# Kernel tuning notes

Hardware: AMD Instinct MI355X
Metric: run time of the kernel (lower is better)

The kernel has to match this reference:

```python
import jax, jax.numpy as jnp
import numpy as np

B, N, K = 2, 32768, 16
D_IN, D_OUT = 8, 32
D_HALF = D_OUT // 2
BLOCK = 1024  # query block size for chunked KNN
EPS = 1e-6    # BatchNorm2d eps in the torch module


def _bn(x, g, b):
    # training-mode BatchNorm over all axes except the trailing channel axis
    axes = tuple(range(x.ndim - 1))
    m = jnp.mean(x, axes, keepdims=True)
    v = jnp.var(x, axes, keepdims=True)
    return (x - m) * jax.lax.rsqrt(v + EPS) * g + b


def _knn_idx(coords, k, block=BLOCK):
    # chunked brute-force KNN: never materializes the full (B,N,N) matrix
    b_, n_, _ = coords.shape
    sq = jnp.sum(coords * coords, -1)  # (B,N)
    q = coords.reshape(b_, n_ // block, block, 3).transpose(1, 0, 2, 3)
    q2 = sq.reshape(b_, n_ // block, block).transpose(1, 0, 2)

    def f(args):
        qi, q2i = args  # (B,block,3), (B,block)
        d = q2i[..., None] + sq[:, None, :] - 2.0 * jnp.einsum('bqc,bnc->bqn', qi, coords)
        return jax.lax.top_k(-d, k)[1]  # (B,block,k) nearest indices

    idx = jax.lax.map(f, (q, q2))  # (nb,B,block,k)
    return idx.transpose(1, 0, 2, 3).reshape(b_, n_, k)


def _lse(coords, feats, idx, Wl, bl, g, b):
    # coords (B,N,3), feats (B,N,C), idx (B,N,K) -> (B,N,K,2C)
    neigh = jax.vmap(lambda c, i: c[i])(coords, idx)            # (B,N,K,3)
    center = jnp.broadcast_to(coords[:, :, None, :], neigh.shape)
    ones = jnp.ones(idx.shape + (1,), coords.dtype)             # torch passes idx only -> dist=1
    cat = jnp.concatenate([center, neigh, center - neigh, ones], -1)  # (B,N,K,10)
    h = jax.nn.relu(_bn(cat @ Wl.T + bl, g, b))                 # (B,N,K,C)
    fexp = jnp.broadcast_to(feats[:, :, None, :], h.shape)
    return jnp.concatenate([h, fexp], -1)


def _attpool(x, Ws, Wp, bp, g, b):
    # x (B,N,K,Cin) -> (B,N,Cout); softmax over K (torch dim=-2 after permute)
    s = jax.nn.softmax(x @ Ws.T, axis=2)
    f = jnp.sum(s * x, 2)                                       # (B,N,Cin)
    return jax.nn.relu(_bn(f @ Wp.T + bp, g, b))


def setup_inputs() -> dict:
    key = jax.random.key(0)
    ks = iter(jax.random.split(key, 40))
    p = lambda *s: jax.random.normal(next(ks), s, jnp.float32) * 0.1
    d = {
        'coords': jax.random.normal(next(ks), (B, N, 3), jnp.float32) * 10.0,
        'features': jax.random.normal(next(ks), (B, D_IN, N, 1), jnp.float32),
        'W1': p(D_HALF, D_IN), 'b1': p(D_HALF),
        'Wl1': p(D_HALF, 10), 'bl1': p(D_HALF),
        'gl1': jnp.ones((D_HALF,), jnp.float32), 'bl1b': jnp.zeros((D_HALF,), jnp.float32),
        'Ws1': p(D_OUT, D_OUT),
        'Wp1': p(D_HALF, D_OUT), 'bp1': p(D_HALF),
        'gp1': jnp.ones((D_HALF,), jnp.float32), 'bp1b': jnp.zeros((D_HALF,), jnp.float32),
        'Wl2': p(D_HALF, 10), 'bl2': p(D_HALF),
        'gl2': jnp.ones((D_HALF,), jnp.float32), 'bl2b': jnp.zeros((D_HALF,), jnp.float32),
        'Ws2': p(D_OUT, D_OUT),
        'Wp2': p(D_OUT, D_OUT), 'bp2': p(D_OUT),
        'gp2': jnp.ones((D_OUT,), jnp.float32), 'bp2b': jnp.zeros((D_OUT,), jnp.float32),
        'W2': p(2 * D_OUT, D_OUT), 'b2': p(2 * D_OUT),
        'Wsc': p(2 * D_OUT, D_IN), 'bsc': p(2 * D_OUT),
        'gsc': jnp.ones((2 * D_OUT,), jnp.float32), 'bscb': jnp.zeros((2 * D_OUT,), jnp.float32),
    }
    return d


def reference(coords, features, W1, b1, Wl1, bl1, gl1, bl1b, Ws1, Wp1, bp1, gp1, bp1b,
              Wl2, bl2, gl2, bl2b, Ws2, Wp2, bp2, gp2, bp2b, W2, b2, Wsc, bsc, gsc, bscb):
    feats = features[:, :, :, 0].transpose(0, 2, 1)             # (B,N,d_in) channel-last
    idx = _knn_idx(jax.lax.stop_gradient(coords), K)            # (B,N,K)
    x = jax.nn.leaky_relu(feats @ W1.T + b1, 0.2)               # mlp1 -> (B,N,d_out/2)
    x = _lse(coords, x, idx, Wl1, bl1, gl1, bl1b)               # (B,N,K,d_out)
    x = _attpool(x, Ws1, Wp1, bp1, gp1, bp1b)                   # (B,N,d_out/2)
    x = _lse(coords, x, idx, Wl2, bl2, gl2, bl2b)               # (B,N,K,d_out)
    x = _attpool(x, Ws2, Wp2, bp2, gp2, bp2b)                   # (B,N,d_out)
    out = x @ W2.T + b2                                         # mlp2 -> (B,N,2*d_out)
    sc = _bn(feats @ Wsc.T + bsc, gsc, bscb)                    # shortcut with BN
    out = jax.nn.leaky_relu(out + sc, 0.01)
    return out.transpose(0, 2, 1)[..., None]                    # (B,2*d_out,N,1)
```

## Files before the change

### kernel.cpp

```cpp
#include <hip/hip_runtime.h>
#include <math.h>

#define NPTS  32768
#define NB    2
#define NQ    (NB*NPTS)
#define KK    16
#define EPS   1e-6f
#define G     16
#define G3    (G*G*G)
#define HB    2048
#define SLOP  0.05f
#define TEPS  1e-3f
#define CAPC  512
#define CAP2  1408
#define INVQK (1.f/(float)((size_t)NQ*KK))
#define INVN  (1.f/(float)NQ)

#define S_L1 0
#define S_L2 32
#define S_P1 64
#define S_P2 96
#define S_SC 160

#define WS_X1     (NQ*16)
#define WS_T2     (NQ*32)
#define WS_T4     (NQ*48)
#define WS_STAT   (NQ*80)
#define WS_COEF   (WS_STAT + 512)
#define WS_GCNT   (WS_STAT + 1024)
#define WS_GSTART (WS_GCNT + 2*G3)
#define WS_CELLID (WS_GSTART + 2*G3)
#define WS_SORTID (WS_CELLID + NQ)
#define WS_CSORT  (WS_SORTID + NQ)
#define WS_BBOX   (WS_CSORT + 4*NQ)
#define WS_HIST   (WS_BBOX + 16)
#define WS_EDGE   (WS_HIST + 6*HB)
#define WS_STARTS WS_HIST
#define WS_FAIL   WS_CELLID
#define WS_PART   WS_CSORT
#define WS_PARTA  WS_T2

#define FB_BAD    (1 << 30)

__device__ __forceinline__ float wred64(float v) {
#pragma unroll
  for (int m = 32; m > 0; m >>= 1) v += __shfl_xor(v, m, 64);
  return v;
}

__device__ __forceinline__ unsigned int encf(float f) {
  unsigned int u = __float_as_uint(f);
  return (u & 0x80000000u) ? ~u : (u | 0x80000000u);
}
__device__ __forceinline__ float decf(unsigned int u) {
  return (u & 0x80000000u) ? __uint_as_float(u & 0x7fffffffu) : __uint_as_float(~u);
}

__device__ __forceinline__ int bs16(const float* e, float x) {
  int c = (x >= e[8]) ? 8 : 0;
  c += (x >= e[c+4]) ? 4 : 0;
  c += (x >= e[c+2]) ? 2 : 0;
  c += (x >= e[c+1]) ? 1 : 0;
  return c;
}

__global__ void k_zero_all(float* __restrict__ stats, int* __restrict__ gcnt,
                           int* __restrict__ hist, unsigned int* __restrict__ bbox,
                           int* __restrict__ failcnt) {
  int i = blockIdx.x*256 + threadIdx.x;
  if (i < 2*G3) gcnt[i] = 0;
  if (i < 6*HB) hist[i] = 0;
  if (i < 320)  stats[i] = 0.f;
  if (i < 12)   bbox[i] = ((i % 6) < 3) ? 0xFFFFFFFFu : 0u;
  if (i == 0)   failcnt[0] = 0;
}

__global__ void k_pred(const float* __restrict__ part, int nblk, int nch,
                       float* __restrict__ stats, int soff) {
  __shared__ float red[256];
  int c = blockIdx.x, tid = threadIdx.x;
  float s = 0.f;
  for (int i = tid; i < nblk; i += 256) s += part[(size_t)i*nch + c];
  red[tid] = s;
  __syncthreads();
  for (int off2 = 128; off2 > 0; off2 >>= 1) {
    if (tid < off2) red[tid] += red[tid + off2];
    __syncthreads();
  }
  if (tid == 0) stats[soff + c] = red[0];
}

__global__ void k_pred2(const float* __restrict__ pa, const float* __restrict__ pb,
                        float* __restrict__ stats) {
  __shared__ float red[256];
  int cb = blockIdx.x, tid = threadIdx.x;
  const float* part; int nblk, nch, soff, c;
  if (cb < 128) { part = pa; nblk = 64;   nch = 128; soff = S_SC; c = cb; }
  else          { part = pb; nblk = 1024; nch = 64;  soff = S_L1; c = cb - 128; }
  float s = 0.f;
  for (int i = tid; i < nblk; i += 256) s += part[(size_t)i*nch + c];
  red[tid] = s;
  __syncthreads();
  for (int off2 = 128; off2 > 0; off2 >>= 1) {
    if (tid < off2) red[tid] += red[tid + off2];
    __syncthreads();
  }
  if (tid == 0) stats[soff + c] = red[0];
}

__global__ void k_bbox(const float* __restrict__ coords, unsigned int* __restrict__ bbox) {
  __shared__ unsigned int rmn[3][4], rmx[3][4];
  int tid = threadIdx.x;
  int t = blockIdx.x*256 + tid;
  int b = t >> 15, n = t & (NPTS-1);
  const float* cb = coords + (size_t)b*(NPTS*3);
  unsigned int e[3] = { encf(cb[n*3+0]), encf(cb[n*3+1]), encf(cb[n*3+2]) };
  unsigned int mn[3] = { e[0], e[1], e[2] }, mx[3] = { e[0], e[1], e[2] };
#pragma unroll
  for (int s = 32; s > 0; s >>= 1) {
#pragma unroll
    for (int a = 0; a < 3; ++a) {
      unsigned int o1 = (unsigned int)__shfl_xor((int)mn[a], s, 64);
      unsigned int o2 = (unsigned int)__shfl_xor((int)mx[a], s, 64);
      mn[a] = mn[a] < o1 ? mn[a] : o1;
      mx[a] = mx[a] > o2 ? mx[a] : o2;
    }
  }
  int wave = tid >> 6, lane = tid & 63;
  if (lane == 0) {
#pragma unroll
    for (int a = 0; a < 3; ++a) { rmn[a][wave] = mn[a]; rmx[a][wave] = mx[a]; }
  }
  __syncthreads();
  if (tid < 3) {
    unsigned int a0 = min(min(rmn[tid][0], rmn[tid][1]), min(rmn[tid][2], rmn[tid][3]));
    unsigned int A0 = max(max(rmx[tid][0], rmx[tid][1]), max(rmx[tid][2], rmx[tid][3]));
    atomicMin(&bbox[b*6 + tid], a0);
    atomicMax(&bbox[b*6 + 3 + tid], A0);
  }
}

__global__ void k_hist(const float* __restrict__ coords, const unsigned int* __restrict__ bbox,
                       int* __restrict__ hist) {
  int t = blockIdx.x*256 + threadIdx.x;
  int b = t >> 15, n = t & (NPTS-1);
  const float* cb = coords + (size_t)b*(NPTS*3);
#pragma unroll
  for (int a = 0; a < 3; ++a) {
    float l = decf(bbox[b*6+a]), h = decf(bbox[b*6+3+a]);
    float ex = (h - l)*(1.f + 4e-7f) + 1e-30f;
    float inv = (float)HB/ex;
    int bin = (int)((cb[n*3+a] - l)*inv);
    bin = min(HB-1, max(0, bin));
    atomicAdd(&hist[(b*3+a)*HB + bin], 1);
  }
}

__global__ void k_edges(const int* __restrict__ hist, const unsigned int* __restrict__ bbox,
                        float* __restrict__ edges) {
  __shared__ int part[256];
  int p = blockIdx.x;
  int b = p/3, a = p - b*3;
  int tid = threadIdx.x;
  const int* h = hist + p*HB;
  int v[8]; int s = 0;
#pragma unroll
  for (int i = 0; i < 8; ++i) { v[i] = h[tid*8 + i]; s += v[i]; }
  part[tid] = s;
  __syncthreads();
  for (int off = 1; off < 256; off <<= 1) {
    int x = part[tid];
    int y = (tid >= off) ? part[tid-off] : 0;
    __syncthreads();
    part[tid] = x + y;
    __syncthreads();
  }
  float l = decf(bbox[b*6+a]), hi = decf(bbox[b*6+3+a]);
  float ex = (hi - l)*(1.f + 4e-7f) + 1e-30f;
  float bw = ex*(1.f/(float)HB);
  int c = part[tid] - s;
#pragma unroll
  for (int i = 0; i < 8; ++i) {
    int lo_c = c; c += v[i];
#pragma unroll
    for (int g = 1; g < G; ++g) {
      int tq = g*(NPTS/G);
      if (lo_c < tq && c >= tq) edges[p*(G+1) + g] = l + bw*(float)(tid*8 + i + 1);
    }
  }
  if (tid == 0) { edges[p*(G+1)] = l; edges[p*(G+1) + G] = hi + fabsf(hi)*1e-6f + 1e-20f; }
}

__global__ void k_bin(const float* __restrict__ coords, const float* __restrict__ edges,
                      int* __restrict__ cellid, int* __restrict__ gcnt) {
  __shared__ float se[3][G+1];
  int tid = threadIdx.x;
  int t = blockIdx.x*256 + tid;
  int b = t >> 15, n = t & (NPTS-1);
  if (tid < 3*(G+1)) se[tid/(G+1)][tid%(G+1)] = edges[b*3*(G+1) + tid];
  __syncthreads();
  const float* cb = coords + (size_t)b*(NPTS*3);
  int c0 = bs16(se[0], cb[n*3+0]);
  int c1 = bs16(se[1], cb[n*3+1]);
  int c2 = bs16(se[2], cb[n*3+2]);
  int cid = b*G3 + (c2*G + c1)*G + c0;
  cellid[t] = cid;
  atomicAdd(&gcnt[cid], 1);
}

__global__ void k_alloc(const int* __restrict__ gcnt, int* __restrict__ gstart,
                        int* __restrict__ starts) {
  __shared__ int part[1024];
  int tid = threadIdx.x;
  int v[8]; int s = 0;
#pragma unroll
  for (int i = 0; i < 8; ++i) { v[i] = gcnt[tid*8 + i]; s += v[i]; }
  part[tid] = s;
  __syncthreads();
  for (int off = 1; off < 1024; off <<= 1) {
    int x = part[tid];
    int y = (tid >= off) ? part[tid-off] : 0;
    __syncthreads();
    part[tid] = x + y;
    __syncthreads();
  }
  int base = part[tid] - s;
#pragma unroll
  for (int i = 0; i < 8; ++i) { gstart[tid*8 + i] = base; starts[tid*8 + i] = base; base += v[i]; }
  if (tid == 1023) starts[2*G3] = NQ;
}

__global__ void k_scatter(const float* __restrict__ coords, const int* __restrict__ cellid,
                          int* __restrict__ gstart, float4* __restrict__ csort,
                          int* __restrict__ sortid) {
  int t = blockIdx.x*256 + threadIdx.x;
  int b = t >> 15, n = t & (NPTS-1);
  const float* cb = coords + (size_t)b*(NPTS*3);
  int cid = cellid[t];
  int pos = atomicAdd(&gstart[cid], 1);
  float x = cb[n*3+0], y = cb[n*3+1], z = cb[n*3+2];
  csort[pos] = make_float4(x, y, z, x*x + y*y + z*z);
  sortid[pos] = n;
}

__launch_bounds__(256)
__global__ void k_cellknn(const float4* __restrict__ csort, const int* __restrict__ sortid,
                          const int* __restrict__ starts, const float* __restrict__ edges,
                          int* __restrict__ oidx, int* __restrict__ faillist,
                          int* __restrict__ failcnt) {
  __shared__ float4 big[CAP2];
  __shared__ float  sbdA[4][64];
  __shared__ int    sbiA[4][64];
  __shared__ int    rs[9], rl[9], pre[10];
  __shared__ int    rs2[25], rl2[25], pre2[26];
  __shared__ int    nfl[4];
  __shared__ int    flq[4][16];
  __shared__ float  flT[4][16];
  int tid = threadIdx.x, lane = tid & 63, w = tid >> 6;
  int blk = blockIdx.x;
  int b = blk >> 12;
  int c = blk & (G3-1);
  int cxi = c & 15, cyi = (c >> 4) & 15, czi = c >> 8;
  const int* st = starts + b*G3;
  float* sbd = &sbdA[w][0];
  int*   sbi = &sbiA[w][0];
  if (tid < 4) nfl[tid] = 0;
  if (tid < 9) {
    int dz = tid/3 - 1, dy = tid%3 - 1;
    int z = czi + dz, y = cyi + dy;
    if (z < 0 || z > G-1 || y < 0 || y > G-1) { rs[tid] = 0; rl[tid] = 0; }
    else {
      int xa = max(cxi-1, 0), xb = min(cxi+1, G-1);
      int c0 = (z*G + y)*G + xa;
      int s0 = st[c0], e0 = st[c0 + (xb - xa) + 1];
      rs[tid] = s0; rl[tid] = e0 - s0;
    }
  }
  __syncthreads();
  if (tid == 0) {
    int acc = 0;
#pragma unroll
    for (int i = 0; i < 9; ++i) { pre[i] = acc; acc += rl[i]; }
    pre[9] = acc;
  }
  __syncthreads();
  int total = pre[9];
  int hs = st[c], he = st[c+1];
  int nq = he - hs;
  if (nq == 0) return;
  bool bad = (total > CAPC) || (total < KK);
  if (!bad) {
    for (int i = tid; i < total; i += 256) {
      int row = 0;
#pragma unroll
      for (int rr = 1; rr < 9; ++rr) row += (i >= pre[rr]);
      int gp = rs[row] + (i - pre[row]);
      big[i] = csort[gp];
    }
  }
  __syncthreads();
  int hoff = pre[4] + (hs - rs[4]);
  float blo[3], bhi[3]; bool blok[3], bhik[3];
  int cc3[3] = {cxi, cyi, czi};
#pragma unroll
  for (int a = 0; a < 3; ++a) {
    const float* e = edges + (b*3 + a)*(G+1);
    blok[a] = cc3[a] > 0;     blo[a] = blok[a] ? e[cc3[a]-1] : 0.f;
    bhik[a] = cc3[a] < G-1;   bhi[a] = bhik[a] ? e[cc3[a]+2] : 0.f;
  }
  for (int q0 = 0; q0 < nq; q0 += 4) {
    int qi = q0 + w;
    if (qi >= nq) continue;
    int t = hs + qi;
    if (bad) {
      if (lane == 0) { int pos = atomicAdd(failcnt, 1); faillist[pos] = t | FB_BAD; }
      continue;
    }
    float4 qv = big[hoff + qi];
    float qx = qv.x, qy = qv.y, qz = qv.z, qsq = qv.w;
    float dreg[8];
#pragma unroll
    for (int s = 0; s < 8; ++s) {
      int i = s*64 + lane;
      float d = 1e30f;
      if (i < total) {
        float4 p = big[i];
        d = qsq + p.w - 2.f*(qx*p.x + qy*p.y + qz*p.z);
      }
      dreg[s] = d;
    }
    float mnl = fminf(fminf(fminf(dreg[0],dreg[1]), fminf(dreg[2],dreg[3])),
                      fminf(fminf(dreg[4],dreg[5]), fminf(dreg[6],dreg[7])));
    float v = mnl;
#pragma unroll
    for (int k2 = 2; k2 <= 64; k2 <<= 1) {
#pragma unroll
      for (int j = k2 >> 1; j > 0; j >>= 1) {
        float o = __shfl_xor(v, j, 64);
        bool keepmin = (((lane & j) == 0) == ((lane & k2) == 0));
        v = keepmin ? fminf(v, o) : fmaxf(v, o);
      }
    }
    float Tp = __shfl(v, 15, 64);
    int cnt = 0;
#pragma unroll
    for (int s = 0; s < 8; ++s) {
      bool take = dreg[s] <= Tp;
      unsigned long long bal = __ballot(take);
      int pos = cnt + __popcll(bal & ((1ull << lane) - 1ull));
      if (take && pos < 64) { sbd[pos] = dreg[s]; sbi[pos] = s*64 + lane; }
      cnt += __popcll(bal);
    }
    if (cnt > 64) {
      if (lane == 0) { int pos = atomicAdd(failcnt, 1); faillist[pos] = t | FB_BAD; }
      continue;
    }
    float dv = (lane < cnt) ? sbd[lane] : 1e30f;
    int   iv = (lane < cnt) ? sbi[lane] : 0x7fffffff;
    if (cnt <= 32) {
#pragma unroll
      for (int kk = 2; kk <= 32; kk <<= 1) {
#pragma unroll
        for (int j = kk >> 1; j > 0; j >>= 1) {
          float od = __shfl_xor(dv, j, 64);
          int   oi = __shfl_xor(iv, j, 64);
          bool keepmin = (((lane & j) == 0) == ((lane & kk) == 0));
          bool less = (od < dv) || (od == dv && oi < iv);
          bool take2 = keepmin ? less : !less;
          dv = take2 ? od : dv;
          iv = take2 ? oi : iv;
        }
      }
    } else {
#pragma unroll
      for (int kk = 2; kk <= 64; kk <<= 1) {
#pragma unroll
        for (int j = kk >> 1; j > 0; j >>= 1) {
          float od = __shfl_xor(dv, j, 64);
          int   oi = __shfl_xor(iv, j, 64);
          bool keepmin = (((lane & j) == 0) == ((lane & kk) == 0));
          bool less = (od < dv) || (od == dv && oi < iv);
          bool take2 = keepmin ? less : !less;
          dv = take2 ? od : dv;
          iv = take2 ? oi : iv;
        }
      }
    }
    float d16v = __shfl(dv, 15, 64);
    int resid = iv;
    float m = 1e30f;
    if (blok[0]) m = fminf(m, qx - blo[0]);
    if (bhik[0]) m = fminf(m, bhi[0] - qx);
    if (blok[1]) m = fminf(m, qy - blo[1]);
    if (bhik[1]) m = fminf(m, bhi[1] - qy);
    if (blok[2]) m = fminf(m, qz - blo[2]);
    if (bhik[2]) m = fminf(m, bhi[2] - qz);
    bool ok = (m > 0.f) && (m*m > d16v + SLOP);
    if (ok) {
      int qn = sortid[t];
      size_t row = ((size_t)(b*NPTS + qn))*KK;
      if (lane < KK) {
        int rowi = 0;
#pragma unroll
        for (int rr = 1; rr < 9; ++rr) rowi += (resid >= pre[rr]);
        int gp = rs[rowi] + (resid - pre[rowi]);
        oidx[row + lane] = sortid[gp];
      }
    } else {
      if (lane == 0) {
        int k2 = nfl[w];
        if (k2 < 16) { flq[w][k2] = t; flT[w][k2] = d16v; nfl[w] = k2 + 1; }
        else { int pos = atomicAdd(failcnt, 1); faillist[pos] = t | FB_BAD; }
      }
    }
  }
  __syncthreads();
  if (bad) return;
  if (nfl[0] + nfl[1] + nfl[2] + nfl[3] == 0) return;

  if (tid < 25) {
    int dz = tid/5 - 2, dy = tid%5 - 2;
    int z = czi + dz, y = cyi + dy;
    if (z < 0 || z > G-1 || y < 0 || y > G-1) { rs2[tid] = 0; rl2[tid] = 0; }
    else {
      int xa = max(cxi-2, 0), xb = min(cxi+2, G-1);
      int c0 = (z*G + y)*G + xa;
      int s0 = st[c0], e0 = st[c0 + (xb - xa) + 1];
      rs2[tid] = s0; rl2[tid] = e0 - s0;
    }
  }
  __syncthreads();
  if (tid == 0) {
    int acc = 0;
#pragma unroll
    for (int i = 0; i < 25; ++i) { pre2[i] = acc; acc += rl2[i]; }
    pre2[25] = acc;
  }
  __syncthreads();
  int total2 = pre2[25];
  if (total2 > CAP2) {
    if (lane == 0) {
      for (int k2 = 0; k2 < nfl[w]; ++k2) {
        int pos = atomicAdd(failcnt, 1); faillist[pos] = flq[w][k2] | FB_BAD;
      }
    }
    return;
  }
  for (int i = tid; i < total2; i += 256) {
    int rowi = 0;
#pragma unroll
    for (int rr = 1; rr < 25; ++rr) rowi += (i >= pre2[rr]);
    int gp = rs2[rowi] + (i - pre2[rowi]);
    big[i] = csort[gp];
  }
  __syncthreads();
  float blo2[3], bhi2[3]; bool blok2[3], bhik2[3];
#pragma unroll
  for (int a = 0; a < 3; ++a) {
    const float* e = edges + (b*3 + a)*(G+1);
    blok2[a] = cc3[a] > 1;     blo2[a] = blok2[a] ? e[cc3[a]-2] : 0.f;
    bhik2[a] = cc3[a] < G-2;   bhi2[a] = bhik2[a] ? e[cc3[a]+3] : 0.f;
  }
  for (int k2 = 0; k2 < nfl[w]; ++k2) {
    int t = flq[w][k2];
    float T0 = flT[w][k2] + TEPS;
    float4 qv = csort[t];
    float qx = qv.x, qy = qv.y, qz = qv.z, qsq = qv.w;
    int cnt = 0;
    for (int base2 = 0; base2 < total2; base2 += 64) {
      int i = base2 + lane;
      bool valid = i < total2;
      float d = 1e30f;
      if (valid) {
        float4 p = big[i];
        d = qsq + p.w - 2.f*(qx*p.x + qy*p.y + qz*p.z);
      }
      bool take = valid && (d <= T0);
      unsigned long long bal = __ballot(take);
      int pos = cnt + __popcll(bal & ((1ull << lane) - 1ull));
      if (take && pos < 64) { sbd[pos] = d; sbi[pos] = i; }
      cnt += __popcll(bal);
    }
    if (cnt > 64) {
      if (lane == 0) { int pos = atomicAdd(failcnt, 1); faillist[pos] = t | FB_BAD; }
      continue;
    }
    float dv = (lane < cnt) ? sbd[lane] : 1e30f;
    int   iv = (lane < cnt) ? sbi[lane] : 0x7fffffff;
#pragma unroll
    for (int kk = 2; kk <= 64; kk <<= 1) {
#pragma unroll
      for (int j = kk >> 1; j > 0; j >>= 1) {
        float od = __shfl_xor(dv, j, 64);
        int   oi = __shfl_xor(iv, j, 64);
        bool keepmin = (((lane & j) == 0) == ((lane & kk) == 0));
        bool less = (od < dv) || (od == dv && oi < iv);
        bool take2 = keepmin ? less : !less;
        dv = take2 ? od : dv;
        iv = take2 ? oi : iv;
      }
    }
    float d16b = __shfl(dv, 15, 64);
    float m = 1e30f;
    if (blok2[0]) m = fminf(m, qx - blo2[0]);
    if (bhik2[0]) m = fminf(m, bhi2[0] - qx);
    if (blok2[1]) m = fminf(m, qy - blo2[1]);
    if (bhik2[1]) m = fminf(m, bhi2[1] - qy);
    if (blok2[2]) m = fminf(m, qz - blo2[2]);
    if (bhik2[2]) m = fminf(m, bhi2[2] - qz);
    bool ok = (m > 0.f) && (m*m > d16b + SLOP);
    int qn = sortid[t];
    size_t row = ((size_t)(b*NPTS + qn))*KK;
    if (lane < KK) {
      int rowi = 0;
#pragma unroll
      for (int rr = 1; rr < 25; ++rr) rowi += (iv >= pre2[rr]);
      int gp = rs2[rowi] + (iv - pre2[rowi]);
      oidx[row + lane] = ok ? sortid[gp] : gp;
    }
    if (!ok && lane == 0) { int pos = atomicAdd(failcnt, 1); faillist[pos] = t; }
  }
}

__launch_bounds__(256)
__global__ void k_knn_fb(const float4* __restrict__ csort, const int* __restrict__ sortid,
                         const int* __restrict__ starts, const float* __restrict__ edges,
                         const int* __restrict__ faillist, const int* __restrict__ failcnt,
                         int* __restrict__ oidx) {
  int tid = threadIdx.x, lane = tid & 63, w = tid >> 6;
  int gw = blockIdx.x*4 + w, nw = gridDim.x*4;
  int nf = failcnt[0];
  for (int f = gw; f < nf; f += nw) {
    int fv = faillist[f];
    bool seeded = (fv & FB_BAD) == 0;
    int t = fv & (FB_BAD - 1);
    int b = t >> 15;
    const int* st = starts + b*G3;
    const float* ex = edges + (b*3+0)*(G+1);
    const float* ey = edges + (b*3+1)*(G+1);
    const float* ez = edges + (b*3+2)*(G+1);
    float4 qv = csort[t];
    const float qx = qv.x, qy = qv.y, qz = qv.z, qsq = qv.w;
    int qn = sortid[t];
    size_t row = ((size_t)(b*NPTS + qn))*KK;
    float T;
    int lo_pos, hi_pos;
    if (seeded) {
      float sd = -1e30f;
      if (lane < KK) {
        int pos = oidx[row + lane];
        float4 p = csort[pos];
        sd = qsq + p.w - 2.f*(qx*p.x + qy*p.y + qz*p.z);
      }
      T = sd;
#pragma unroll
      for (int m = 32; m > 0; m >>= 1) T = fmaxf(T, __shfl_xor(T, m, 64));
      T += TEPS;
      float R = sqrtf(T)*1.0001f + 1e-12f;
      bool tk = (lane < G-1) && (ex[lane+1] < qx - R);
      int xl = __popcll(__ballot(tk));
      tk = (lane >= 1 && lane <= G-1) && (ex[lane] > qx + R);
      int xh = (G-1) - __popcll(__ballot(tk));
      tk = (lane < G-1) && (ey[lane+1] < qy - R);
      int yl = __popcll(__ballot(tk));
      tk = (lane >= 1 && lane <= G-1) && (ey[lane] > qy + R);
      int yh = (G-1) - __popcll(__ballot(tk));
      tk = (lane < G-1) && (ez[lane+1] < qz - R);
      int zl = __popcll(__ballot(tk));
      tk = (lane >= 1 && lane <= G-1) && (ez[lane] > qz + R);
      int zh = (G-1) - __popcll(__ballot(tk));
      lo_pos = st[(zl*G + yl)*G + xl];
      hi_pos = st[(zh*G + yh)*G + xh + 1];
    } else {
      float mn = 1e30f;
      for (int i = b*NPTS + lane; i < b*NPTS + NPTS; i += 64) {
        float4 p = csort[i];
        float d = qsq + p.w - 2.f*(qx*p.x + qy*p.y + qz*p.z);
        mn = fminf(mn, d);
      }
      float v = mn;
#pragma unroll
      for (int k2 = 2; k2 <= 64; k2 <<= 1) {
#pragma unroll
        for (int j = k2 >> 1; j > 0; j >>= 1) {
          float o = __shfl_xor(v, j, 64);
          bool keepmin = (((lane & j) == 0) == ((lane & k2) == 0));
          v = keepmin ? fminf(v, o) : fmaxf(v, o);
        }
      }
      T = __shfl(v, 15, 64) + TEPS;
      lo_pos = b*NPTS;
      hi_pos = b*NPTS + NPTS;
    }
    float dl[KK]; int il[KK];
#pragma unroll
    for (int i = 0; i < KK; ++i) { dl[i] = 1e30f; il[i] = 0x7fffffff; }
    for (int i = lo_pos + lane; i < hi_pos; i += 64) {
      float4 p = csort[i];
      float d = qsq + p.w - 2.f*(qx*p.x + qy*p.y + qz*p.z);
      if (d <= T && d < dl[KK-1]) {
        float cd = d; int ci = i;
#pragma unroll
        for (int i2 = 0; i2 < KK; ++i2) {
          bool sw = cd < dl[i2];
          float td = dl[i2]; int ti = il[i2];
          dl[i2] = sw ? cd : td; il[i2] = sw ? ci : ti;
          cd = sw ? td : cd;    ci = sw ? ti : ci;
        }
      }
    }
    int res = 0;
#pragma unroll
    for (int r = 0; r < KK; ++r) {
      float v = dl[0]; int pi = il[0]; int l = lane;
#pragma unroll
      for (int m = 1; m < 64; m <<= 1) {
        float ov = __shfl_xor(v, m, 64);
        int   op = __shfl_xor(pi, m, 64);
        int   ol = __shfl_xor(l, m, 64);
        bool take = (ov < v) || (ov == v && op < pi);
        v = take ? ov : v; pi = take ? op : pi; l = take ? ol : l;
      }
      if (lane == r) res = pi;
      bool win = (lane == l);
#pragma unroll
      for (int i = 0; i < KK-1; ++i) {
        dl[i] = win ? dl[i+1] : dl[i];
        il[i] = win ? il[i+1] : il[i];
      }
      dl[KK-1] = win ? 1e30f : dl[KK-1];
      il[KK-1] = win ? 0x7fffffff : il[KK-1];
    }
    if (lane < KK) oidx[row + lane] = sortid[res];
  }
}

__global__ void k_stats(const float* __restrict__ features,
                        const float* __restrict__ W1, const float* __restrict__ b1,
                        const float* __restrict__ Wsc, const float* __restrict__ bsc,
                        float* __restrict__ x1, float* __restrict__ ppa,
                        const float* __restrict__ coords, const int* __restrict__ idx,
                        const float* __restrict__ Wl1, const float* __restrict__ bl1,
                        const float* __restrict__ Wl2, const float* __restrict__ bl2,
                        float* __restrict__ ppb) {
  int tid = threadIdx.x;
  if (blockIdx.x < 64) {
    __shared__ float sW1[128], sb1[16], sWsc[512], sbsc[64];
    __shared__ float part[128];
    if (tid < 128) { sW1[tid] = W1[tid]; part[tid] = 0.f; }
    if (tid < 16)  sb1[tid] = b1[tid];
    if (tid < 64)  sbsc[tid] = bsc[tid];
    for (int i = tid; i < 512; i += 256) sWsc[i] = Wsc[i];
    __syncthreads();
    int q0 = blockIdx.x*1024;
    float f[4][8];
#pragma unroll
    for (int p = 0; p < 4; ++p) {
      int q = q0 + p*256 + tid;
      int b = q >> 15, n = q & (NPTS-1);
#pragma unroll
      for (int c = 0; c < 8; ++c) f[p][c] = features[((size_t)b*8 + c)*NPTS + n];
#pragma unroll
      for (int co = 0; co < 16; ++co) {
        float a = sb1[co];
#pragma unroll
        for (int c = 0; c < 8; ++c) a += f[p][c]*sW1[co*8+c];
        x1[(size_t)q*16 + co] = a > 0.f ? a : 0.2f*a;
      }
    }
    int lane = tid & 63;
#pragma unroll
    for (int co = 0; co < 64; ++co) {
      float s = 0.f, ss = 0.f;
#pragma unroll
      for (int p = 0; p < 4; ++p) {
        float a = sbsc[co];
#pragma unroll
        for (int c = 0; c < 8; ++c) a += f[p][c]*sWsc[co*8+c];
        s += a; ss += a*a;
      }
      s = wred64(s); ss = wred64(ss);
      if (lane == 0) { atomicAdd(&part[co], s); atomicAdd(&part[64+co], ss); }
    }
    __syncthreads();
    if (tid < 128) ppa[(size_t)blockIdx.x*128 + tid] = part[tid];
  } else {
    __shared__ float sW1[160], sb1[16], sW2[160], sb2[16];
    __shared__ float red[4][64];
    int blk = blockIdx.x - 64;
    for (int i = tid; i < 160; i += 256) { sW1[i] = Wl1[i]; sW2[i] = Wl2[i]; }
    if (tid < 16) { sb1[tid] = bl1[tid]; sb2[tid] = bl2[tid]; }
    __syncthreads();
    float cat[4][10];
#pragma unroll
    for (int p = 0; p < 4; ++p) {
      int t = blk*1024 + p*256 + tid;
      int q = t >> 4;
      int b = q >> 15, n = q & (NPTS-1);
      const float* cb = coords + (size_t)b*(NPTS*3);
      int j = idx[t];
      float cx = cb[n*3], cy = cb[n*3+1], cz = cb[n*3+2];
      float px = cb[j*3], py = cb[j*3+1], pz = cb[j*3+2];
      cat[p][0]=cx; cat[p][1]=cy; cat[p][2]=cz;
      cat[p][3]=px; cat[p][4]=py; cat[p][5]=pz;
      cat[p][6]=cx-px; cat[p][7]=cy-py; cat[p][8]=cz-pz; cat[p][9]=1.f;
    }
    int wave = tid >> 6, lane = tid & 63;
#pragma unroll
    for (int co = 0; co < 16; ++co) {
      float s1 = 0.f, q1 = 0.f, s2 = 0.f, q2 = 0.f;
#pragma unroll
      for (int p = 0; p < 4; ++p) {
        float a1 = sb1[co], a2 = sb2[co];
#pragma unroll
        for (int d0 = 0; d0 < 10; ++d0) { a1 += cat[p][d0]*sW1[co*10+d0]; a2 += cat[p][d0]*sW2[co*10+d0]; }
        s1 += a1; q1 += a1*a1; s2 += a2; q2 += a2*a2;
      }
      s1 = wred64(s1); q1 = wred64(q1);
      s2 = wred64(s2); q2 = wred64(q2);
      if (lane == 0) { red[wave][co]=s1; red[wave][16+co]=q1; red[wave][32+co]=s2; red[wave][48+co]=q2; }
    }
    __syncthreads();
    if (tid < 64) {
      float v = red[0][tid] + red[1][tid] + red[2][tid] + red[3][tid];
      ppb[(size_t)blk*64 + tid] = v;
    }
  }
}

__launch_bounds__(256)
__global__ void k_att1(const float* __restrict__ coords, const int* __restrict__ idx,
                       const float* __restrict__ x1ws,
                       const float* __restrict__ Wl1, const float* __restrict__ bl1,
                       const float* __restrict__ Ws1, const float* __restrict__ Wp1,
                       const float* __restrict__ bp1, const float* __restrict__ stats,
                       const float* __restrict__ gl1, const float* __restrict__ bl1b,
                       float* __restrict__ t2, float* __restrict__ ppart) {
  __shared__ float saL[16], scL[16];
  __shared__ float sWl[160], sbl[16];
  __shared__ float sWs[1024];
  __shared__ float sWpT[512], sbp[16];
  __shared__ float lsum[16], lsq[16];
  int tid = threadIdx.x;
  if (tid < 16) {
    float m = stats[S_L1 + tid]*INVQK;
    float v = stats[S_L1 + 16 + tid]*INVQK - m*m;
    float a = gl1[tid]*rsqrtf(v + EPS);
    saL[tid] = a; scL[tid] = bl1b[tid] - m*a;
  }
  __syncthreads();
  for (int i = tid; i < 160; i += 256) { int c = i/10; sWl[i] = Wl1[i]*saL[c]; }
  if (tid < 16) sbl[tid] = bl1[tid]*saL[tid] + scL[tid];
  for (int i = tid; i < 1024; i += 256) sWs[i] = Ws1[i];
  for (int i = tid; i < 512; i += 256) { int co = i >> 4, cp = i & 15; sWpT[i] = Wp1[cp*32 + co]; }
  if (tid < 16) { sbp[tid] = bp1[tid]; lsum[tid] = 0.f; lsq[tid] = 0.f; }
  __syncthreads();
  int gp = blockIdx.x*16 + (tid >> 4);
  int k  = tid & 15;
  int b = gp >> 15, n = gp & (NPTS-1);
  const float* cb = coords + (size_t)b*(NPTS*3);
  int j = idx[(size_t)gp*KK + k];
  float cx = cb[n*3], cy = cb[n*3+1], cz = cb[n*3+2];
  float px = cb[j*3], py = cb[j*3+1], pz = cb[j*3+2];
  float cat[10] = {cx,cy,cz,px,py,pz,cx-px,cy-py,cz-pz,1.f};
  float x[32];
#pragma unroll
  for (int co = 0; co < 16; ++co) {
    float a = sbl[co];
#pragma unroll
    for (int d0 = 0; d0 < 10; ++d0) a += cat[d0]*sWl[co*10+d0];
    x[co] = a > 0.f ? a : 0.f;
  }
  {
    const float4* xp = (const float4*)(x1ws + (size_t)gp*16);
    float4 u0 = xp[0], u1 = xp[1], u2 = xp[2], u3 = xp[3];
    x[16]=u0.x; x[17]=u0.y; x[18]=u0.z; x[19]=u0.w;
    x[20]=u1.x; x[21]=u1.y; x[22]=u1.z; x[23]=u1.w;
    x[24]=u2.x; x[25]=u2.y; x[26]=u2.z; x[27]=u2.w;
    x[28]=u3.x; x[29]=u3.y; x[30]=u3.z; x[31]=u3.w;
  }
  float tacc = sbp[k];
#pragma unroll
  for (int co = 0; co < 32; ++co) {
    float s = 0.f;
#pragma unroll
    for (int ci = 0; ci < 32; ++ci) s += x[ci]*sWs[co*32+ci];
    float e = __expf(s);
    float se = e;
#pragma unroll
    for (int msk = 8; msk > 0; msk >>= 1) se += __shfl_xor(se, msk, 16);
    float w = e/se;
    float fv = w*x[co];
#pragma unroll
    for (int msk = 8; msk > 0; msk >>= 1) fv += __shfl_xor(fv, msk, 16);
    tacc += fv*sWpT[co*16+k];
  }
  t2[(size_t)gp*16 + k] = tacc;
  atomicAdd(&lsum[k], tacc);
  atomicAdd(&lsq[k], tacc*tacc);
  __syncthreads();
  if (tid < 16) {
    ppart[(size_t)blockIdx.x*32 + tid]      = lsum[tid];
    ppart[(size_t)blockIdx.x*32 + 16 + tid] = lsq[tid];
  }
}

__launch_bounds__(256)
__global__ void k_att2(const float* __restrict__ coords, const int* __restrict__ idx,
                       const float* __restrict__ t2ws,
                       const float* __restrict__ Wl2, const float* __restrict__ bl2,
                       const float* __restrict__ Ws2, const float* __restrict__ Wp2,
                       const float* __restrict__ bp2, const float* __restrict__ stats,
                       const float* __restrict__ gl2, const float* __restrict__ bl2b,
                       const float* __restrict__ gp1, const float* __restrict__ bp1b,
                       float* __restrict__ t4, float* __restrict__ ppart) {
  __shared__ float saL[16], scL[16];
  __shared__ float sWl[160], sbl[16];
  __shared__ float sWs[1024];
  __shared__ float sWpT[1024], sbp[32];
  __shared__ float sa1[16], sc1[16];
  __shared__ float lsum[32], lsq[32];
  int tid = threadIdx.x;
  if (tid < 16) {
    float m = stats[S_L2 + tid]*INVQK;
    float v = stats[S_L2 + 16 + tid]*INVQK - m*m;
    float a = gl2[tid]*rsqrtf(v + EPS);
    saL[tid] = a; scL[tid] = bl2b[tid] - m*a;
    float m1 = stats[S_P1 + tid]*INVN;
    float v1 = stats[S_P1 + 16 + tid]*INVN - m1*m1;
    float a1 = gp1[tid]*rsqrtf(v1 + EPS);
    sa1[tid] = a1; sc1[tid] = bp1b[tid] - m1*a1;
  }
  __syncthreads();
  for (int i = tid; i < 160; i += 256) { int c = i/10; sWl[i] = Wl2[i]*saL[c]; }
  if (tid < 16) sbl[tid] = bl2[tid]*saL[tid] + scL[tid];
  for (int i = tid; i < 1024; i += 256) {
    sWs[i] = Ws2[i];
    int co = i >> 5, cp = i & 31; sWpT[i] = Wp2[cp*32 + co];
  }
  if (tid < 32) { sbp[tid] = bp2[tid]; lsum[tid]=0.f; lsq[tid]=0.f; }
  __syncthreads();
  int gp = blockIdx.x*16 + (tid >> 4);
  int k  = tid & 15;
  int b = gp >> 15, n = gp & (NPTS-1);
  const float* cb = coords + (size_t)b*(NPTS*3);
  int j = idx[(size_t)gp*KK + k];
  float cx = cb[n*3], cy = cb[n*3+1], cz = cb[n*3+2];
  float px = cb[j*3], py = cb[j*3+1], pz = cb[j*3+2];
  float cat[10] = {cx,cy,cz,px,py,pz,cx-px,cy-py,cz-pz,1.f};
  float x[32];
#pragma unroll
  for (int co = 0; co < 16; ++co) {
    float a = sbl[co];
#pragma unroll
    for (int d0 = 0; d0 < 10; ++d0) a += cat[d0]*sWl[co*10+d0];
    x[co] = a > 0.f ? a : 0.f;
  }
  {
    const float4* xp = (const float4*)(t2ws + (size_t)gp*16);
    float4 u0 = xp[0], u1 = xp[1], u2 = xp[2], u3 = xp[3];
    float xv[16] = {u0.x,u0.y,u0.z,u0.w, u1.x,u1.y,u1.z,u1.w,
                    u2.x,u2.y,u2.z,u2.w, u3.x,u3.y,u3.z,u3.w};
#pragma unroll
    for (int c = 0; c < 16; ++c) {
      float v = xv[c]*sa1[c] + sc1[c];
      x[16+c] = v > 0.f ? v : 0.f;
    }
  }
  float tacc0 = sbp[k], tacc1 = sbp[k+16];
#pragma unroll
  for (int co = 0; co < 32; ++co) {
    float s = 0.f;
#pragma unroll
    for (int ci = 0; ci < 32; ++ci) s += x[ci]*sWs[co*32+ci];
    float e = __expf(s);
    float se = e;
#pragma unroll
    for (int msk = 8; msk > 0; msk >>= 1) se += __shfl_xor(se, msk, 16);
    float w = e/se;
    float fv = w*x[co];
#pragma unroll
    for (int msk = 8; msk > 0; msk >>= 1) fv += __shfl_xor(fv, msk, 16);
    tacc0 += fv*sWpT[co*32+k];
    tacc1 += fv*sWpT[co*32+k+16];
  }
  t4[(size_t)gp*32 + k]      = tacc0;
  t4[(size_t)gp*32 + k + 16] = tacc1;
  atomicAdd(&lsum[k], tacc0);      atomicAdd(&lsq[k], tacc0*tacc0);
  atomicAdd(&lsum[k+16], tacc1);   atomicAdd(&lsq[k+16], tacc1*tacc1);
  __syncthreads();
  if (tid < 32) {
    ppart[(size_t)blockIdx.x*64 + tid]      = lsum[tid];
    ppart[(size_t)blockIdx.x*64 + 32 + tid] = lsq[tid];
  }
}

__global__ void k_final(const float* __restrict__ t4ws, const float* __restrict__ features,
                        const float* __restrict__ W2, const float* __restrict__ b2,
                        const float* __restrict__ Wsc, const float* __restrict__ bsc,
                        const float* __restrict__ stats,
                        const float* __restrict__ gsc, const float* __restrict__ bscb,
                        const float* __restrict__ gp2, const float* __restrict__ bp2b,
                        float* __restrict__ out) {
  __shared__ float saS[64], scS[64];
  __shared__ float sW2[2048], sb2[64], sWscF[512], sbscF[64], sa[32], scc[32];
  int tid = threadIdx.x;
  if (tid < 64) {
    float m = stats[S_SC + tid]*INVN;
    float v = stats[S_SC + 64 + tid]*INVN - m*m;
    float a = gsc[tid]*rsqrtf(v + EPS);
    saS[tid] = a; scS[tid] = bscb[tid] - m*a;
  }
  if (tid < 32) {
    float m = stats[S_P2 + tid]*INVN;
    float v = stats[S_P2 + 32 + tid]*INVN - m*m;
    float a = gp2[tid]*rsqrtf(v + EPS);
    sa[tid] = a; scc[tid] = bp2b[tid] - m*a;
  }
  __syncthreads();
  for (int i = tid; i < 2048; i += 256) sW2[i] = W2[i];
  if (tid < 64) sb2[tid] = b2[tid];
  for (int i = tid; i < 512; i += 256) { int c2 = i >> 3; sWscF[i] = Wsc[i]*saS[c2]; }
  if (tid < 64) sbscF[tid] = bsc[tid]*saS[tid] + scS[tid];
  __syncthreads();
  int q = blockIdx.x*256 + tid;
  int b = q >> 15, n = q & (NPTS-1);
  float x3[32];
  const float4* tp = (const float4*)(t4ws + (size_t)q*32);
#pragma unroll
  for (int i = 0; i < 8; ++i) {
    float4 u = tp[i];
    float v0 = u.x*sa[4*i+0] + scc[4*i+0];
    float v1 = u.y*sa[4*i+1] + scc[4*i+1];
    float v2 = u.z*sa[4*i+2] + scc[4*i+2];
    float v3 = u.w*sa[4*i+3] + scc[4*i+3];
    x3[4*i+0] = v0 > 0.f ? v0 : 0.f;
    x3[4*i+1] = v1 > 0.f ? v1 : 0.f;
    x3[4*i+2] = v2 > 0.f ? v2 : 0.f;
    x3[4*i+3] = v3 > 0.f ? v3 : 0.f;
  }
  float f[8];
#pragma unroll
  for (int c = 0; c < 8; ++c) f[c] = features[((size_t)b*8+c)*NPTS + n];
  for (int c2 = 0; c2 < 64; ++c2) {
    float acc = sb2[c2];
#pragma unroll
    for (int co = 0; co < 32; ++co) acc += x3[co]*sW2[c2*32+co];
    float sv = sbscF[c2];
#pragma unroll
    for (int c = 0; c < 8; ++c) sv += f[c]*sWscF[c2*8+c];
    float o = acc + sv;
    out[((size_t)b*64 + c2)*NPTS + n] = o > 0.f ? o : 0.01f*o;
  }
}

extern "C" void kernel_launch(void* const* d_in, const int* in_sizes, int n_in,
                              void* d_out, int out_size, void* d_ws, size_t ws_size,
                              hipStream_t stream) {
  const float* coords   = (const float*)d_in[0];
  const float* features = (const float*)d_in[1];
  const float* W1  = (const float*)d_in[2];
  const float* b1  = (const float*)d_in[3];
  const float* Wl1 = (const float*)d_in[4];
  const float* bl1 = (const float*)d_in[5];
  const float* gl1 = (const float*)d_in[6];
  const float* bl1b= (const float*)d_in[7];
  const float* Ws1 = (const float*)d_in[8];
  const float* Wp1 = (const float*)d_in[9];
  const float* bp1 = (const float*)d_in[10];
  const float* gp1 = (const float*)d_in[11];
  const float* bp1b= (const float*)d_in[12];
  const float* Wl2 = (const float*)d_in[13];
  const float* bl2 = (const float*)d_in[14];
  const float* gl2 = (const float*)d_in[15];
  const float* bl2b= (const float*)d_in[16];
  const float* Ws2 = (const float*)d_in[17];
  const float* Wp2 = (const float*)d_in[18];
  const float* bp2 = (const float*)d_in[19];
  const float* gp2 = (const float*)d_in[20];
  const float* bp2b= (const float*)d_in[21];
  const float* W2  = (const float*)d_in[22];
  const float* b2  = (const float*)d_in[23];
  const float* Wsc = (const float*)d_in[24];
  const float* bsc = (const float*)d_in[25];
  const float* gsc = (const float*)d_in[26];
  const float* bscb= (const float*)d_in[27];

  float* wsF  = (float*)d_ws;
  int*   wsI  = (int*)d_ws;
  int*   idxp = wsI;
  float* x1p  = wsF + WS_X1;
  float* t2p  = wsF + WS_T2;
  float* t4p  = wsF + WS_T4;
  float* stat = wsF + WS_STAT;
  int*   gcnt = wsI + WS_GCNT;
  int*   gsta = wsI + WS_GSTART;
  int*   gcel = wsI + WS_CELLID;
  int*   sid  = wsI + WS_SORTID;
  float4* csrt = (float4*)(wsF + WS_CSORT);
  unsigned int* bbox = (unsigned int*)(wsI + WS_BBOX);
  int*   fcnt = wsI + WS_BBOX + 12;
  int*   flist= wsI + WS_FAIL;
  int*   hist = wsI + WS_HIST;
  int*   strt = wsI + WS_STARTS;
  float* edge = wsF + WS_EDGE;
  float* prt  = wsF + WS_PART;
  float* prtA = wsF + WS_PARTA;
  float* outp = (float*)d_out;

  hipLaunchKernelGGL(k_zero_all, dim3(48), dim3(256), 0, stream, stat, gcnt, hist, bbox, fcnt);
  hipLaunchKernelGGL(k_bbox,    dim3(NQ/256), dim3(256), 0, stream, coords, bbox);
  hipLaunchKernelGGL(k_hist,    dim3(NQ/256), dim3(256), 0, stream, coords, bbox, hist);
  hipLaunchKernelGGL(k_edges,   dim3(6), dim3(256), 0, stream, hist, bbox, edge);
  hipLaunchKernelGGL(k_bin,     dim3(NQ/256), dim3(256), 0, stream, coords, edge, gcel, gcnt);
  hipLaunchKernelGGL(k_alloc,   dim3(1), dim3(1024), 0, stream, gcnt, gsta, strt);
  hipLaunchKernelGGL(k_scatter, dim3(NQ/256), dim3(256), 0, stream, coords, gcel, gsta, csrt, sid);
  hipLaunchKernelGGL(k_cellknn, dim3(2*G3), dim3(256), 0, stream,
                     csrt, sid, strt, edge, idxp, flist, fcnt);
  hipLaunchKernelGGL(k_knn_fb,  dim3(2048), dim3(256), 0, stream,
                     csrt, sid, strt, edge, flist, fcnt, idxp);
  hipLaunchKernelGGL(k_stats, dim3(64 + (NQ*KK)/1024), dim3(256), 0, stream,
                     features, W1, b1, Wsc, bsc, x1p, prtA,
                     coords, idxp, Wl1, bl1, Wl2, bl2, prt);
  hipLaunchKernelGGL(k_pred2, dim3(192), dim3(256), 0, stream, prtA, prt, stat);
  hipLaunchKernelGGL(k_att1, dim3(NQ/16), dim3(256), 0, stream,
                     coords, idxp, x1p, Wl1, bl1, Ws1, Wp1, bp1, stat, gl1, bl1b, t2p, prt);
  hipLaunchKernelGGL(k_pred, dim3(32), dim3(256), 0, stream, prt, NQ/16, 32, stat, S_P1);
  hipLaunchKernelGGL(k_att2, dim3(NQ/16), dim3(256), 0, stream,
                     coords, idxp, t2p, Wl2, bl2, Ws2, Wp2, bp2, stat,
                     gl2, bl2b, gp1, bp1b, t4p, prt);
  hipLaunchKernelGGL(k_pred, dim3(64), dim3(256), 0, stream, prt, NQ/16, 64, stat, S_P2);
  hipLaunchKernelGGL(k_final, dim3(NQ/256), dim3(256), 0, stream,
                     t4p, features, W2, b2, Wsc, bsc, stat, gsc, bscb, gp2, bp2b, outp);
}
```

Before: 709.3 us.

## Process each KNN fallback query with a whole block and merge per-wave top-k

The fallback KNN kernel now assigns one query per 256-thread block instead of one per wavefront. The four waves scan the candidate range with a stride of 256, and their per-wave top-16 lists are merged in shared memory with a bitonic sort in wave 0. For unseeded queries, the separate pass that computed a brute-force min threshold is dropped and the threshold is set to infinity. The intent is to cut per-query latency on long scans, at the cost of block-level barriers and idle waves when candidate ranges are short.

```diff
diff --git a/kernel.cpp b/kernel.cpp
--- a/kernel.cpp
+++ b/kernel.cpp
@@ -527,75 +527,66 @@
                          const int* __restrict__ starts, const float* __restrict__ edges,
                          const int* __restrict__ faillist, const int* __restrict__ failcnt,
                          int* __restrict__ oidx) {
+  __shared__ float sT;
+  __shared__ int   slo, shi;
+  __shared__ float md[64];
+  __shared__ int   mp[64];
   int tid = threadIdx.x, lane = tid & 63, w = tid >> 6;
-  int gw = blockIdx.x*4 + w, nw = gridDim.x*4;
   int nf = failcnt[0];
-  for (int f = gw; f < nf; f += nw) {
+  for (int f = blockIdx.x; f < nf; f += gridDim.x) {
     int fv = faillist[f];
     bool seeded = (fv & FB_BAD) == 0;
     int t = fv & (FB_BAD - 1);
     int b = t >> 15;
     const int* st = starts + b*G3;
-    const float* ex = edges + (b*3+0)*(G+1);
-    const float* ey = edges + (b*3+1)*(G+1);
-    const float* ez = edges + (b*3+2)*(G+1);
     float4 qv = csort[t];
     const float qx = qv.x, qy = qv.y, qz = qv.z, qsq = qv.w;
     int qn = sortid[t];
     size_t row = ((size_t)(b*NPTS + qn))*KK;
-    float T;
-    int lo_pos, hi_pos;
-    if (seeded) {
-      float sd = -1e30f;
-      if (lane < KK) {
-        int pos = oidx[row + lane];
-        float4 p = csort[pos];
-        sd = qsq + p.w - 2.f*(qx*p.x + qy*p.y + qz*p.z);
-      }
-      T = sd;
-#pragma unroll
-      for (int m = 32; m > 0; m >>= 1) T = fmaxf(T, __shfl_xor(T, m, 64));
-      T += TEPS;
-      float R = sqrtf(T)*1.0001f + 1e-12f;
-      bool tk = (lane < G-1) && (ex[lane+1] < qx - R);
-      int xl = __popcll(__ballot(tk));
-      tk = (lane >= 1 && lane <= G-1) && (ex[lane] > qx + R);
-      int xh = (G-1) - __popcll(__ballot(tk));
-      tk = (lane < G-1) && (ey[lane+1] < qy - R);
-      int yl = __popcll(__ballot(tk));
-      tk = (lane >= 1 && lane <= G-1) && (ey[lane] > qy + R);
-      int yh = (G-1) - __popcll(__ballot(tk));
-      tk = (lane < G-1) && (ez[lane+1] < qz - R);
-      int zl = __popcll(__ballot(tk));
-      tk = (lane >= 1 && lane <= G-1) && (ez[lane] > qz + R);
-      int zh = (G-1) - __popcll(__ballot(tk));
-      lo_pos = st[(zl*G + yl)*G + xl];
-      hi_pos = st[(zh*G + yh)*G + xh + 1];
-    } else {
-      float mn = 1e30f;
-      for (int i = b*NPTS + lane; i < b*NPTS + NPTS; i += 64) {
-        float4 p = csort[i];
-        float d = qsq + p.w - 2.f*(qx*p.x + qy*p.y + qz*p.z);
-        mn = fminf(mn, d);
-      }
-      float v = mn;
-#pragma unroll
-      for (int k2 = 2; k2 <= 64; k2 <<= 1) {
-#pragma unroll
-        for (int j = k2 >> 1; j > 0; j >>= 1) {
-          float o = __shfl_xor(v, j, 64);
-          bool keepmin = (((lane & j) == 0) == ((lane & k2) == 0));
-          v = keepmin ? fminf(v, o) : fmaxf(v, o);
+    if (w == 0) {
+      if (seeded) {
+        const float* ex = edges + (b*3+0)*(G+1);
+        const float* ey = edges + (b*3+1)*(G+1);
+        const float* ez = edges + (b*3+2)*(G+1);
+        float sd = -1e30f;
+        if (lane < KK) {
+          int pos = oidx[row + lane];
+          float4 p = csort[pos];
+          sd = qsq + p.w - 2.f*(qx*p.x + qy*p.y + qz*p.z);
         }
-      }
-      T = __shfl(v, 15, 64) + TEPS;
-      lo_pos = b*NPTS;
-      hi_pos = b*NPTS + NPTS;
-    }
+        float T = sd;
+#pragma unroll
+        for (int m = 32; m > 0; m >>= 1) T = fmaxf(T, __shfl_xor(T, m, 64));
+        T += TEPS;
+        float R = sqrtf(T)*1.0001f + 1e-12f;
+        bool tk = (lane < G-1) && (ex[lane+1] < qx - R);
+        int xl = __popcll(__ballot(tk));
+        tk = (lane >= 1 && lane <= G-1) && (ex[lane] > qx + R);
+        int xh = (G-1) - __popcll(__ballot(tk));
+        tk = (lane < G-1) && (ey[lane+1] < qy - R);
+        int yl = __popcll(__ballot(tk));
+        tk = (lane >= 1 && lane <= G-1) && (ey[lane] > qy + R);
+        int yh = (G-1) - __popcll(__ballot(tk));
+        tk = (lane < G-1) && (ez[lane+1] < qz - R);
+        int zl = __popcll(__ballot(tk));
+        tk = (lane >= 1 && lane <= G-1) && (ez[lane] > qz + R);
+        int zh = (G-1) - __popcll(__ballot(tk));
+        if (lane == 0) {
+          sT = T;
+          slo = st[(zl*G + yl)*G + xl];
+          shi = st[(zh*G + yh)*G + xh + 1];
+        }
+      } else {
+        if (lane == 0) { sT = 1e30f; slo = b*NPTS; shi = b*NPTS + NPTS; }
+      }
+    }
+    __syncthreads();
+    float T = sT;
+    int lo_pos = slo, hi_pos = shi;
     float dl[KK]; int il[KK];
 #pragma unroll
     for (int i = 0; i < KK; ++i) { dl[i] = 1e30f; il[i] = 0x7fffffff; }
-    for (int i = lo_pos + lane; i < hi_pos; i += 64) {
+    for (int i = lo_pos + tid; i < hi_pos; i += 256) {
       float4 p = csort[i];
       float d = qsq + p.w - 2.f*(qx*p.x + qy*p.y + qz*p.z);
       if (d <= T && d < dl[KK-1]) {
@@ -609,7 +600,7 @@
         }
       }
     }
-    int res = 0;
+    int res = 0x7fffffff; float rd = 1e30f;
 #pragma unroll
     for (int r = 0; r < KK; ++r) {
       float v = dl[0]; int pi = il[0]; int l = lane;
@@ -621,7 +612,7 @@
         bool take = (ov < v) || (ov == v && op < pi);
         v = take ? ov : v; pi = take ? op : pi; l = take ? ol : l;
       }
-      if (lane == r) res = pi;
+      if (lane == r) { res = pi; rd = v; }
       bool win = (lane == l);
 #pragma unroll
       for (int i = 0; i < KK-1; ++i) {
@@ -631,7 +622,26 @@
       dl[KK-1] = win ? 1e30f : dl[KK-1];
       il[KK-1] = win ? 0x7fffffff : il[KK-1];
     }
-    if (lane < KK) oidx[row + lane] = sortid[res];
+    if (lane < KK) { md[w*KK + lane] = rd; mp[w*KK + lane] = res; }
+    __syncthreads();
+    if (w == 0) {
+      float dv = md[lane]; int iv = mp[lane];
+#pragma unroll
+      for (int kk = 2; kk <= 64; kk <<= 1) {
+#pragma unroll
+        for (int j = kk >> 1; j > 0; j >>= 1) {
+          float od = __shfl_xor(dv, j, 64);
+          int   oi = __shfl_xor(iv, j, 64);
+          bool keepmin = (((lane & j) == 0) == ((lane & kk) == 0));
+          bool less = (od < dv) || (od == dv && oi < iv);
+          bool take2 = keepmin ? less : !less;
+          dv = take2 ? od : dv;
+          iv = take2 ? oi : iv;
+        }
+      }
+      if (lane < KK) oidx[row + lane] = sortid[iv];
+    }
+    __syncthreads();
   }
 }
 
```

Result: faster. 671.9 us (-5.3%).
